# Kernel tuning notes

Measured on AMD Instinct MI355X. Metric: run time of the kernel, lower is better.

Reference implementation:

```python
import jax, jax.numpy as jnp
import numpy as np

N = 100000          # nodes
E = 1600000         # edges (before self loops)
F_IN = 128          # num_features
HID = 16            # hidden_channels (per head)
HEADS = 4
NCLS = 16           # num_classes (per head)
NEG_SLOPE = 0.2     # PyG GATv2Conv default


def gatv2_conv(x, src, dst, w_l, w_r, att, bias, heads, out_ch):
    """PyG GATv2Conv (concat=True, add_self_loops handled by caller).
    x: [N, Fin]; src/dst: [E']; w_l/w_r: [Fin, heads*out_ch]; att: [heads, out_ch].
    """
    n = x.shape[0]
    x_l = (x @ w_l).reshape(n, heads, out_ch)  # source-side transform
    x_r = (x @ w_r).reshape(n, heads, out_ch)  # target-side transform
    # per-edge attention logits: a^T LeakyReLU(x_l[j] + x_r[i])
    e = jax.nn.leaky_relu(x_l[src] + x_r[dst], NEG_SLOPE)   # [E', H, C]
    logits = jnp.einsum('ehc,hc->eh', e, att)               # [E', H]
    # segment softmax over incoming edges of each dst node
    m = jax.ops.segment_max(logits, dst, num_segments=n)    # [N, H]
    a = jnp.exp(logits - m[dst])
    denom = jax.ops.segment_sum(a, dst, num_segments=n)     # [N, H]
    alpha = a / denom[dst]                                  # self loops => denom > 0
    out = jax.ops.segment_sum(alpha[:, :, None] * x_l[src], dst, num_segments=n)
    return out.reshape(n, heads * out_ch) + bias


def setup_inputs() -> dict:
    key = jax.random.key(0)
    ks = jax.random.split(key, 10)
    x = jax.random.normal(ks[0], (N, F_IN), dtype=jnp.float32)
    edge_index = jax.random.randint(ks[1], (2, E), 0, N, dtype=jnp.int64)
    d1 = HEADS * HID   # 64
    s1 = 1.0 / np.sqrt(F_IN)
    s2 = 1.0 / np.sqrt(d1)
    return {
        'x': x,
        'edge_index': edge_index,
        'w_l1': jax.random.normal(ks[2], (F_IN, d1), dtype=jnp.float32) * s1,
        'w_r1': jax.random.normal(ks[3], (F_IN, d1), dtype=jnp.float32) * s1,
        'att1': jax.random.normal(ks[4], (HEADS, HID), dtype=jnp.float32) * s2,
        'b1': jnp.zeros((d1,), dtype=jnp.float32),
        'w_l2': jax.random.normal(ks[5], (d1, HEADS * NCLS), dtype=jnp.float32) * s2,
        'w_r2': jax.random.normal(ks[6], (d1, HEADS * NCLS), dtype=jnp.float32) * s2,
        'att2': jax.random.normal(ks[7], (HEADS, NCLS), dtype=jnp.float32) * (1.0 / np.sqrt(NCLS)),
        'b2': jnp.zeros((HEADS * NCLS,), dtype=jnp.float32),
    }


def reference(x, edge_index, w_l1, w_r1, att1, b1, w_l2, w_r2, att2, b2):
    # add self loops (PyG GATv2Conv default add_self_loops=True)
    loop = jnp.arange(N, dtype=edge_index.dtype)
    src = jnp.concatenate([edge_index[0], loop])
    dst = jnp.concatenate([edge_index[1], loop])
    h = gatv2_conv(x, src, dst, w_l1, w_r1, att1, b1, HEADS, HID)
    h = jax.nn.relu(h)
    out = gatv2_conv(h, src, dst, w_l2, w_r2, att2, b2, HEADS, NCLS)
    return out
```

## Files before the change

kernel.cpp:

```cpp
#include <hip/hip_runtime.h>
#include <hip/hip_fp16.h>

#define FIN 128
#define BSH 9
#define BMASK ((1 << BSH) - 1)
#define CHUNK 8192
#define BCAP 10240

typedef _Float16 half4 __attribute__((ext_vector_type(4)));
typedef _Float16 h2v __attribute__((ext_vector_type(2)));
typedef float f32x4 __attribute__((ext_vector_type(4)));

template<int K, bool FP32IN>
__global__ __launch_bounds__(256) void gemm_mfma(
    const void* __restrict__ xin, const float* __restrict__ wl,
    const float* __restrict__ wr, __half* __restrict__ outl,
    __half* __restrict__ outr, int n) {
  constexpr int WSTR = K + 4;
  __shared__ _Float16 Wt[128 * WSTR];
  const int tid = threadIdx.x;
  for (int i4 = tid; i4 < K * 16; i4 += 256) {
    const int k = i4 >> 4, c0 = (i4 & 15) << 2;
    const float4 vl = *(const float4*)&wl[k * 64 + c0];
    const float4 vr = *(const float4*)&wr[k * 64 + c0];
    Wt[(c0 + 0) * WSTR + k] = (_Float16)vl.x;
    Wt[(c0 + 1) * WSTR + k] = (_Float16)vl.y;
    Wt[(c0 + 2) * WSTR + k] = (_Float16)vl.z;
    Wt[(c0 + 3) * WSTR + k] = (_Float16)vl.w;
    Wt[(c0 + 64) * WSTR + k] = (_Float16)vr.x;
    Wt[(c0 + 65) * WSTR + k] = (_Float16)vr.y;
    Wt[(c0 + 66) * WSTR + k] = (_Float16)vr.z;
    Wt[(c0 + 67) * WSTR + k] = (_Float16)vr.w;
  }
  __syncthreads();
  const int lane = tid & 63;
  const int wv = tid >> 6;
  const int r0 = blockIdx.x * 64 + wv * 16;
  const int rowc = min(r0 + (lane & 15), n - 1);
  const int kgrp = (lane >> 4) << 2;
  const int col16 = lane & 15;
  f32x4 acc[8];
#pragma unroll
  for (int cf = 0; cf < 8; ++cf) acc[cf] = {0.f, 0.f, 0.f, 0.f};

  for (int ks = 0; ks < K / 16; ++ks) {
    const int kb = ks * 16 + kgrp;
    half4 a;
    if (FP32IN) {
      const float4 av =
          *(const float4*)((const float*)xin + (size_t)rowc * K + kb);
      a = {(_Float16)av.x, (_Float16)av.y, (_Float16)av.z, (_Float16)av.w};
    } else {
      a = *(const half4*)((const __half*)xin + (size_t)rowc * K + kb);
    }
#pragma unroll
    for (int cf = 0; cf < 8; ++cf) {
      const half4 b = *(const half4*)&Wt[(cf * 16 + col16) * WSTR + kb];
      acc[cf] = __builtin_amdgcn_mfma_f32_16x16x16f16(a, b, acc[cf], 0, 0, 0);
    }
  }
  const int crow0 = r0 + ((lane >> 4) << 2);
#pragma unroll
  for (int cf = 0; cf < 8; ++cf) {
    const int c = cf * 16 + col16;
    __half* outp = (c < 64) ? outl : outr;
    const int cc = c & 63;
#pragma unroll
    for (int r = 0; r < 4; ++r) {
      const int rr = crow0 + r;
      if (rr < n) outp[(size_t)rr * 64 + cc] = (__half)acc[cf][r];
    }
  }
}

__global__ void init_misc(int NB, int* __restrict__ gcursor,
                          const float* __restrict__ att1,
                          const float* __restrict__ att2,
                          __half* __restrict__ att1h,
                          __half* __restrict__ att2h) {
  const int t = threadIdx.x;
  if (t < NB) gcursor[t] = t * BCAP;
  if (t < 64) {
    att1h[t] = (__half)(att1[t] * 1.44269504f);
    att2h[t] = (__half)(att2[t] * 1.44269504f);
  }
}

__global__ __launch_bounds__(256) void binpass(
    const int* __restrict__ src, const int* __restrict__ dst, int E, int ET,
    int NB, int* __restrict__ gcursor, unsigned* __restrict__ sorted_val) {
  __shared__ unsigned lval[CHUNK];
  __shared__ unsigned char lb[CHUNK];
  __shared__ int c1[256], c2[256], base[256];
  const int tid = threadIdx.x;
  c1[tid] = 0;
  c2[tid] = 0;
  __syncthreads();
  const int e0 = blockIdx.x * CHUNK;
#pragma unroll
  for (int j = 0; j < CHUNK / 256; ++j) {
    const int idx = tid + 256 * j;
    const int e = e0 + idx;
    if (e < ET) {
      int s, d;
      if (e < E) {
        s = src[e];
        d = dst[e];
      } else {
        s = d = e - E;
      }
      const int b = d >> BSH;
      lval[idx] = (unsigned)s | ((unsigned)(d & BMASK) << 17);
      lb[idx] = (unsigned char)b;
      atomicAdd(&c1[b], 1);
    } else {
      lb[idx] = 255;
    }
  }
  __syncthreads();
  if (tid < NB && c1[tid] > 0) base[tid] = atomicAdd(&gcursor[tid], c1[tid]);
  __syncthreads();
#pragma unroll
  for (int j = 0; j < CHUNK / 256; ++j) {
    const int idx = tid + 256 * j;
    const int b = lb[idx];
    if (b != 255) {
      const int r = atomicAdd(&c2[b], 1);
      sorted_val[base[b] + r] = lval[idx];
    }
  }
}

__global__ __launch_bounds__(256) void bucket_scatter(
    const int* __restrict__ gcursor, const unsigned* __restrict__ sorted_val,
    int n, int* __restrict__ ssrc, int* __restrict__ off_beg,
    int* __restrict__ off_end) {
  __shared__ int cnt[512], sa[512], sb[512], cur[512];
  __shared__ int buf[BCAP];
  const int b = blockIdx.x;
  const int tid = threadIdx.x;
  const int node0 = b << BSH;
  const int nn = min(512, n - node0);
  const int rbase = b * BCAP;
  const int rlen = gcursor[b] - rbase;
  for (int j = tid; j < 512; j += 256) cnt[j] = 0;
  __syncthreads();
  for (int i = tid; i < rlen; i += 256)
    atomicAdd(&cnt[sorted_val[rbase + i] >> 17], 1);
  __syncthreads();
  for (int j = tid; j < 512; j += 256) sa[j] = cnt[j];
  __syncthreads();
  int* pin = sa;
  int* pout = sb;
  for (int off = 1; off < 512; off <<= 1) {
    for (int j = tid; j < 512; j += 256)
      pout[j] = pin[j] + (j >= off ? pin[j - off] : 0);
    __syncthreads();
    int* t = pin;
    pin = pout;
    pout = t;
  }
  for (int j = tid; j < 512; j += 256) {
    const int excl = pin[j] - cnt[j];
    cur[j] = excl;
    if (j < nn) {
      off_beg[node0 + j] = rbase + excl;
      off_end[node0 + j] = rbase + pin[j];
    }
  }
  __syncthreads();
  if (rlen <= BCAP) {
    for (int i = tid; i < rlen; i += 256) {
      const unsigned v = sorted_val[rbase + i];
      const int p = atomicAdd(&cur[v >> 17], 1);
      buf[p] = (int)(v & 0x1FFFFu);
    }
    __syncthreads();
    for (int i = tid; i < rlen; i += 256) ssrc[rbase + i] = buf[i];
  } else {
    for (int i = tid; i < rlen; i += 256) {
      const unsigned v = sorted_val[rbase + i];
      const int p = atomicAdd(&cur[v >> 17], 1);
      ssrc[rbase + p] = (int)(v & 0x1FFFFu);
    }
  }
}

template<bool RELU, typename OT>
__global__ __launch_bounds__(256) void node_pass(
    const int* __restrict__ off_beg, const int* __restrict__ off_end,
    const int* __restrict__ ssrc, const __half* __restrict__ xl,
    const __half* __restrict__ xr, const __half* __restrict__ atth,
    const float* __restrict__ bias, OT* __restrict__ out, int n) {
  const int lane = threadIdx.x & 63;
  const int grp = lane >> 3;
  const int sl = lane & 7;
  const int d = (blockIdx.x * blockDim.x + threadIdx.x) >> 6;
  if (d >= n) return;
  const int beg = off_beg[d], end = off_end[d];
  const int deg = end - beg;

  union H8 { float4 f4; h2v h2[4]; uint4 u4; };
  H8 ath;
  ath.u4 = *(const uint4*)&atth[8 * sl];
  H8 xrv;
  xrv.f4 = *(const float4*)&xr[(size_t)d * 64 + 8 * sl];

  float acc[8] = {0.f, 0.f, 0.f, 0.f, 0.f, 0.f, 0.f, 0.f};
  float den = 0.f;

  const __half* xlp = xl + 8 * sl;
  const int sv = ssrc[min(beg + lane, end - 1)];

#define EDGE_CORE(vreg_)                                                     \
  {                                                                          \
    H8 ul;                                                                   \
    ul.f4 = (vreg_);                                                         \
    float p = 0.f;                                                           \
    _Pragma("unroll") for (int q = 0; q < 4; ++q) {                          \
      const h2v t = ul.h2[q] + xrv.h2[q];                                    \
      const h2v lk = __builtin_elementwise_max(t, t * (_Float16)0.2f);       \
      p = __builtin_amdgcn_fdot2(lk, ath.h2[q], p, false);                   \
    }                                                                        \
    p += __shfl_xor(p, 1);                                                   \
    const float a = exp2f(p);                                                \
    _Pragma("unroll") for (int q = 0; q < 4; ++q) {                          \
      acc[2 * q] += a * (float)ul.h2[q].x;                                   \
      acc[2 * q + 1] += a * (float)ul.h2[q].y;                               \
    }                                                                        \
    den += a;                                                                \
  }

  if (deg <= 40) {
#define XLF(base_, dst_)                                                     \
  {                                                                          \
    const int s_ = __shfl(sv, (base_) - beg + grp);                          \
    dst_ = *(const float4*)&xlp[(size_t)s_ * 64];                            \
  }
    float4 a0, a1, nx;
    XLF(beg, a0);
    XLF(beg + 8, a1);
    int base = beg;
#pragma unroll 2
    for (; base + 8 <= end; base += 8) {
      XLF(base + 16, nx);
      EDGE_CORE(a0);
      a0 = a1;
      a1 = nx;
    }
    if (base < end) {
      if (base + grp < end) EDGE_CORE(a0);
    }
#undef XLF
  } else {
#define XLS(base_, dst_)                                                     \
  {                                                                          \
    const int idx_ = (base_) - beg + grp;                                    \
    int s_ = __shfl(sv, idx_ & 63);                                          \
    if (idx_ >= 64) s_ = ssrc[min((base_) + grp, end - 1)];                  \
    dst_ = *(const float4*)&xlp[(size_t)s_ * 64];                            \
  }
    float4 a0, a1, nx;
    XLS(beg, a0);
    XLS(beg + 8, a1);
    for (int base = beg; base < end; base += 8) {
      XLS(base + 16, nx);
      if (base + grp < end) EDGE_CORE(a0);
      a0 = a1;
      a1 = nx;
    }
#undef XLS
  }
#undef EDGE_CORE

#pragma unroll
  for (int m = 8; m <= 32; m <<= 1) {
#pragma unroll
    for (int q = 0; q < 8; ++q) acc[q] += __shfl_xor(acc[q], m);
    den += __shfl_xor(den, m);
  }
  if (grp == 0) {
    const float4 b0 = *(const float4*)&bias[8 * sl];
    const float4 b1 = *(const float4*)&bias[8 * sl + 4];
    const float inv = 1.0f / den;
    float v[8];
    v[0] = acc[0] * inv + b0.x;
    v[1] = acc[1] * inv + b0.y;
    v[2] = acc[2] * inv + b0.z;
    v[3] = acc[3] * inv + b0.w;
    v[4] = acc[4] * inv + b1.x;
    v[5] = acc[5] * inv + b1.y;
    v[6] = acc[6] * inv + b1.z;
    v[7] = acc[7] * inv + b1.w;
    if (RELU) {
#pragma unroll
      for (int q = 0; q < 8; ++q) v[q] = fmaxf(v[q], 0.f);
    }
    if constexpr (sizeof(OT) == 2) {
      union { uint4 u; __half2 h[4]; } o;
#pragma unroll
      for (int q = 0; q < 4; ++q)
        o.h[q] = __floats2half2_rn(v[2 * q], v[2 * q + 1]);
      *(uint4*)&out[(size_t)d * 64 + 8 * sl] = o.u;
    } else {
      const float4 o0 = {v[0], v[1], v[2], v[3]};
      const float4 o1 = {v[4], v[5], v[6], v[7]};
      *(float4*)&out[(size_t)d * 64 + 8 * sl] = o0;
      *(float4*)&out[(size_t)d * 64 + 8 * sl + 4] = o1;
    }
  }
}

extern "C" void kernel_launch(void* const* d_in, const int* in_sizes, int n_in,
                              void* d_out, int out_size, void* d_ws, size_t ws_size,
                              hipStream_t stream) {
  const float* x    = (const float*)d_in[0];
  const int*   ei   = (const int*)d_in[1];
  const float* wl1  = (const float*)d_in[2];
  const float* wr1  = (const float*)d_in[3];
  const float* att1 = (const float*)d_in[4];
  const float* b1   = (const float*)d_in[5];
  const float* wl2  = (const float*)d_in[6];
  const float* wr2  = (const float*)d_in[7];
  const float* att2 = (const float*)d_in[8];
  const float* b2   = (const float*)d_in[9];
  float* out = (float*)d_out;

  const int n = in_sizes[0] / FIN;
  const int E = in_sizes[1] / 2;
  const int ET = E + n;
  const int* src = ei;
  const int* dst = ei + E;
  const int NB = (n + (1 << BSH) - 1) >> BSH;

  __half* A  = (__half*)d_ws;
  __half* B  = A + (size_t)n * 64;
  __half* Hh = B + (size_t)n * 64;
  __half* att1h = Hh + (size_t)n * 64;
  __half* att2h = att1h + 64;
  int* off_beg = (int*)(att2h + 64);
  int* off_end = off_beg + n;
  int* gcursor = off_end + n;
  unsigned* sorted_val = (unsigned*)(gcursor + 256);
  int* ssrc = (int*)(sorted_val + (size_t)NB * BCAP);

  const int nbin = (ET + CHUNK - 1) / CHUNK;

  init_misc<<<1, 256, 0, stream>>>(NB, gcursor, att1, att2, att1h, att2h);
  binpass<<<nbin, 256, 0, stream>>>(src, dst, E, ET, NB, gcursor, sorted_val);
  bucket_scatter<<<NB, 256, 0, stream>>>(gcursor, sorted_val, n, ssrc,
                                         off_beg, off_end);

  const int gb = (n + 63) / 64;
  const int nb = (n * 64 + 255) / 256;

  gemm_mfma<128, true><<<gb, 256, 0, stream>>>(x, wl1, wr1, A, B, n);
  node_pass<true, __half><<<nb, 256, 0, stream>>>(off_beg, off_end, ssrc, A, B,
                                                  att1h, b1, Hh, n);

  gemm_mfma<64, false><<<gb, 256, 0, stream>>>(Hh, wl2, wr2, A, B, n);
  node_pass<false, float><<<nb, 256, 0, stream>>>(off_beg, off_end, ssrc, A, B,
                                                  att2h, b2, out, n);
}
```

Baseline: 175.0 us.

## Use DPP swap, fdot2 accumulation, and LDS-based cross-group reduction in node pass

Replaces the xor-1 shuffle with a DPP quad-permute move and folds the per-edge weighted accumulation into fdot2 instructions using half-precision attention weights. The final 8-group reduction of 8 accumulators via 24 shuffles is replaced by writing partials to shared memory and having each lane sum one output column, so all 64 lanes store one element. This cuts cross-lane shuffle traffic and ALU work. In exchange it rounds attention weights to fp16 and adds LDS traffic. The shared-memory read happens without a barrier, which relies on a single wavefront executing in lockstep.

New measurement: 163.9 us. 6.3% less time.

```diff
diff --git a/kernel.cpp b/kernel.cpp
--- a/kernel.cpp
+++ b/kernel.cpp
@@ -10,6 +10,12 @@
 typedef _Float16 half4 __attribute__((ext_vector_type(4)));
 typedef _Float16 h2v __attribute__((ext_vector_type(2)));
 typedef float f32x4 __attribute__((ext_vector_type(4)));
+
+static __device__ __forceinline__ float xor1_add(float p) {
+  const int sw = __builtin_amdgcn_mov_dpp(__builtin_bit_cast(int, p), 0xB1,
+                                          0xF, 0xF, true);
+  return p + __builtin_bit_cast(float, sw);
+}
 
 template<int K, bool FP32IN>
 __global__ __launch_bounds__(256) void gemm_mfma(
@@ -192,7 +198,9 @@
     const int* __restrict__ ssrc, const __half* __restrict__ xl,
     const __half* __restrict__ xr, const __half* __restrict__ atth,
     const float* __restrict__ bias, OT* __restrict__ out, int n) {
+  __shared__ float part[4][8][64];
   const int lane = threadIdx.x & 63;
+  const int wv = threadIdx.x >> 6;
   const int grp = lane >> 3;
   const int sl = lane & 7;
   const int d = (blockIdx.x * blockDim.x + threadIdx.x) >> 6;
@@ -222,11 +230,15 @@
       const h2v lk = __builtin_elementwise_max(t, t * (_Float16)0.2f);       \
       p = __builtin_amdgcn_fdot2(lk, ath.h2[q], p, false);                   \
     }                                                                        \
-    p += __shfl_xor(p, 1);                                                   \
+    p = xor1_add(p);                                                         \
     const float a = exp2f(p);                                                \
+    const _Float16 ah = (_Float16)a;                                         \
+    const h2v aL = {ah, (_Float16)0.f};                                      \
+    const h2v aH = {(_Float16)0.f, ah};                                      \
     _Pragma("unroll") for (int q = 0; q < 4; ++q) {                          \
-      acc[2 * q] += a * (float)ul.h2[q].x;                                   \
-      acc[2 * q + 1] += a * (float)ul.h2[q].y;                               \
+      acc[2 * q] = __builtin_amdgcn_fdot2(ul.h2[q], aL, acc[2 * q], false);  \
+      acc[2 * q + 1] =                                                       \
+          __builtin_amdgcn_fdot2(ul.h2[q], aH, acc[2 * q + 1], false);       \
     }                                                                        \
     den += a;                                                                \
   }
@@ -274,41 +286,19 @@
 #undef EDGE_CORE
 
 #pragma unroll
-  for (int m = 8; m <= 32; m <<= 1) {
-#pragma unroll
-    for (int q = 0; q < 8; ++q) acc[q] += __shfl_xor(acc[q], m);
-    den += __shfl_xor(den, m);
-  }
-  if (grp == 0) {
-    const float4 b0 = *(const float4*)&bias[8 * sl];
-    const float4 b1 = *(const float4*)&bias[8 * sl + 4];
-    const float inv = 1.0f / den;
-    float v[8];
-    v[0] = acc[0] * inv + b0.x;
-    v[1] = acc[1] * inv + b0.y;
-    v[2] = acc[2] * inv + b0.z;
-    v[3] = acc[3] * inv + b0.w;
-    v[4] = acc[4] * inv + b1.x;
-    v[5] = acc[5] * inv + b1.y;
-    v[6] = acc[6] * inv + b1.z;
-    v[7] = acc[7] * inv + b1.w;
-    if (RELU) {
-#pragma unroll
-      for (int q = 0; q < 8; ++q) v[q] = fmaxf(v[q], 0.f);
-    }
-    if constexpr (sizeof(OT) == 2) {
-      union { uint4 u; __half2 h[4]; } o;
-#pragma unroll
-      for (int q = 0; q < 4; ++q)
-        o.h[q] = __floats2half2_rn(v[2 * q], v[2 * q + 1]);
-      *(uint4*)&out[(size_t)d * 64 + 8 * sl] = o.u;
-    } else {
-      const float4 o0 = {v[0], v[1], v[2], v[3]};
-      const float4 o1 = {v[4], v[5], v[6], v[7]};
-      *(float4*)&out[(size_t)d * 64 + 8 * sl] = o0;
-      *(float4*)&out[(size_t)d * 64 + 8 * sl + 4] = o1;
-    }
-  }
+  for (int m = 8; m <= 32; m <<= 1) den += __shfl_xor(den, m);
+  const float den_c = __shfl(den, (lane >> 4) << 1);
+
+  *(float4*)&part[wv][grp][8 * sl] = make_float4(acc[0], acc[1], acc[2], acc[3]);
+  *(float4*)&part[wv][grp][8 * sl + 4] =
+      make_float4(acc[4], acc[5], acc[6], acc[7]);
+  float s = 0.f;
+#pragma unroll
+  for (int g = 0; g < 8; ++g) s += part[wv][g][lane];
+
+  float v = s / den_c + bias[lane];
+  if (RELU) v = fmaxf(v, 0.f);
+  out[(size_t)d * 64 + lane] = (OT)v;
 }
 
 extern "C" void kernel_launch(void* const* d_in, const int* in_sizes, int n_in,
```
